# Optimization experiments

Measured on AMD Instinct MI355X. Metric: run time of the kernel, lower is better.

## Reference

```python
import jax, jax.numpy as jnp
import numpy as np

M, N, T = 32, 32, 512
H1 = (M + N) * 10 * 8      # 5120
H2 = M * N * 4             # 4096
HID = 1000                 # GRU hidden (hardcoded in module)
EPS = 1e-12


def _l2norm(x):
    # torch.nn.functional.normalize: x / max(||x||_2, eps)
    return x / jnp.maximum(jnp.linalg.norm(x), EPS)


def setup_inputs() -> dict:
    key = jax.random.key(0)
    ks = jax.random.split(key, 16)
    rn = lambda k, shp, s: (jax.random.normal(k, shp, dtype=jnp.float32) * s)
    inp = {
        "y": rn(ks[0], (T, N), 1.0),
        "F": rn(ks[1], (M, M), 0.5 / np.sqrt(M)),   # stable dynamics
        "H": rn(ks[2], (N, M), 1.0 / np.sqrt(M)),
        "m1x0": rn(ks[3], (M,), 1.0),
        "h0": rn(ks[4], (HID,), 1.0),
        "W1": rn(ks[5], (H1, M + N), 1.0 / np.sqrt(M + N)),
        "b1": rn(ks[6], (H1,), 0.01),
        "Wih": rn(ks[7], (3 * HID, H1), 1.0 / np.sqrt(H1)),
        "bih": rn(ks[8], (3 * HID,), 0.01),
        "Whh": rn(ks[9], (3 * HID, HID), 1.0 / np.sqrt(HID)),
        "bhh": rn(ks[10], (3 * HID,), 0.01),
        "W2": rn(ks[11], (H2, HID), 1.0 / np.sqrt(HID)),
        "b2": rn(ks[12], (H2,), 0.01),
        "W3": rn(ks[13], (M * N, H2), 1.0 / np.sqrt(H2)),
        "b3": rn(ks[14], (M * N,), 0.01),
    }
    return inp


def reference(y, F, H, m1x0, h0, W1, b1, Wih, bih, Whh, bhh, W2, b2, W3, b3):
    m, n = F.shape[0], H.shape[0]

    def step(carry, yt):
        m1x_prior, m1x_post, h = carry
        # step_prior
        m1x_prev_prior = m1x_prior
        m1x_prior = F @ m1x_post              # [m]
        m1y = H @ m1x_prior                   # [n]
        # step_KGain_est: features
        dm1x_n = _l2norm(m1x_post - m1x_prev_prior)
        dm1y_n = _l2norm(yt - m1y)
        kin = jnp.concatenate([dm1y_n, dm1x_n])  # [n+m]
        # KGain_step: Linear+ReLU -> single-step GRU -> Linear+ReLU -> Linear
        x = jax.nn.relu(W1 @ kin + b1)        # [H1]
        gi = Wih @ x + bih                    # [3*HID]
        gh = Whh @ h + bhh
        ir, iz, ic = jnp.split(gi, 3)
        hr, hz, hc = jnp.split(gh, 3)
        r = jax.nn.sigmoid(ir + hr)
        z = jax.nn.sigmoid(iz + hz)
        c = jnp.tanh(ic + r * hc)
        h_new = (1.0 - z) * c + z * h         # GRU hidden [HID]
        l2 = jax.nn.relu(W2 @ h_new + b2)     # [H2]
        KG = (W3 @ l2 + b3).reshape(m, n)     # Kalman gain
        # KNet_step: innovation update
        m1x_post_new = m1x_prior + KG @ (yt - m1y)
        return (m1x_prior, m1x_post_new, h_new), m1x_post_new

    init = (m1x0, m1x0, h0)
    _, posts = jax.lax.scan(step, init, y)
    return posts  # [T, m]
```

## Files before the change

### kernel.cpp

```cpp
#include <hip/hip_runtime.h>
#include <cmath>

#define Mdim 32
#define Ndim 32
#define Tsteps 512
#define H1dim 5120
#define H2dim 4096
#define HIDdim 1000
#define NWG 256
#define NTHR 1024
#define POLLER 320

typedef unsigned int u32;
typedef unsigned short u16;
typedef unsigned int u32x4 __attribute__((ext_vector_type(4)));

__device__ u16 g_w2b[H2dim * HIDdim];
__device__ u16 g_w3t[H2dim * Mdim * Ndim];

#define OFF_WIH 0
#define OFF_WHH 122880
#define OFF_UNION 146880
#define OFF_H9 157120
#define OFF_MISC 161640
#define SMEM_BYTES 162560

#define MI_POST 0
#define MI_PRIOR 32
#define MI_INNOV 96
#define MI_KIN 128
#define MI_GI 192
#define MI_GH 204

#define BAR_ARR(g) ((g) * 32)
#define BAR_L2 1024
#define BAR_GO(g) (2048 + (g) * 32)

__device__ __forceinline__ u16 f2bf(float f) {
  u32 u = __float_as_uint(f);
  return (u16)((u + 0x7fffu + ((u >> 16) & 1u)) >> 16);
}
__device__ __forceinline__ float bflo(u32 u) { return __uint_as_float(u << 16); }
__device__ __forceinline__ float bfhi(u32 u) { return __uint_as_float(u & 0xffff0000u); }

__device__ __forceinline__ float dot4(float4 a, float4 b) {
  return a.x * b.x + a.y * b.y + a.z * b.z + a.w * b.w;
}
__device__ __forceinline__ float dot8_bb(uint4 a, uint4 b) {
  float s = 0.f;
  s = fmaf(bflo(a.x), bflo(b.x), s); s = fmaf(bfhi(a.x), bfhi(b.x), s);
  s = fmaf(bflo(a.y), bflo(b.y), s); s = fmaf(bfhi(a.y), bfhi(b.y), s);
  s = fmaf(bflo(a.z), bflo(b.z), s); s = fmaf(bfhi(a.z), bfhi(b.z), s);
  s = fmaf(bflo(a.w), bflo(b.w), s); s = fmaf(bfhi(a.w), bfhi(b.w), s);
  return s;
}
__device__ __forceinline__ float dot8_bf(uint4 a, const float* x8) {
  float s = 0.f;
  s = fmaf(bflo(a.x), x8[0], s); s = fmaf(bfhi(a.x), x8[1], s);
  s = fmaf(bflo(a.y), x8[2], s); s = fmaf(bfhi(a.y), x8[3], s);
  s = fmaf(bflo(a.z), x8[4], s); s = fmaf(bfhi(a.z), x8[5], s);
  s = fmaf(bflo(a.w), x8[6], s); s = fmaf(bfhi(a.w), x8[7], s);
  return s;
}

__device__ __forceinline__ float wave_reduce64(float v) {
#pragma unroll
  for (int off = 32; off >= 1; off >>= 1) v += __shfl_xor(v, off, 64);
  return v;
}

__device__ __forceinline__ uint4 ldg_cg4u(const void* p) {
  uint4 r;
  asm volatile("global_load_dwordx4 %0, %1, off sc0 sc1\n\ts_waitcnt vmcnt(0)"
               : "=v"(r) : "v"(p) : "memory");
  return r;
}
__device__ __forceinline__ void stg_cg4u(void* p, u32 a, u32 b, u32 c, u32 d) {
  u32x4 v; v.x = a; v.y = b; v.z = c; v.w = d;
  asm volatile("global_store_dwordx4 %0, %1, off sc0 sc1" :: "v"(p), "v"(v) : "memory");
}
__device__ __forceinline__ void stg_cg1u(u32* p, u32 v) {
  asm volatile("global_store_dword %0, %1, off sc0 sc1" :: "v"(p), "v"(v) : "memory");
}
__device__ __forceinline__ float ldg_sum16_cg(const float* p) {
  float r0, r1, r2, r3, r4, r5, r6, r7, r8, r9, r10, r11, r12, r13, r14, r15;
  asm volatile(
      "global_load_dword %0, %16, off sc0 sc1\n\t"
      "global_load_dword %1, %16, off offset:128 sc0 sc1\n\t"
      "global_load_dword %2, %16, off offset:256 sc0 sc1\n\t"
      "global_load_dword %3, %16, off offset:384 sc0 sc1\n\t"
      "global_load_dword %4, %16, off offset:512 sc0 sc1\n\t"
      "global_load_dword %5, %16, off offset:640 sc0 sc1\n\t"
      "global_load_dword %6, %16, off offset:768 sc0 sc1\n\t"
      "global_load_dword %7, %16, off offset:896 sc0 sc1\n\t"
      "global_load_dword %8, %16, off offset:1024 sc0 sc1\n\t"
      "global_load_dword %9, %16, off offset:1152 sc0 sc1\n\t"
      "global_load_dword %10, %16, off offset:1280 sc0 sc1\n\t"
      "global_load_dword %11, %16, off offset:1408 sc0 sc1\n\t"
      "global_load_dword %12, %16, off offset:1536 sc0 sc1\n\t"
      "global_load_dword %13, %16, off offset:1664 sc0 sc1\n\t"
      "global_load_dword %14, %16, off offset:1792 sc0 sc1\n\t"
      "global_load_dword %15, %16, off offset:1920 sc0 sc1\n\t"
      "s_waitcnt vmcnt(0)"
      : "=&v"(r0), "=&v"(r1), "=&v"(r2), "=&v"(r3), "=&v"(r4), "=&v"(r5),
        "=&v"(r6), "=&v"(r7), "=&v"(r8), "=&v"(r9), "=&v"(r10), "=&v"(r11),
        "=&v"(r12), "=&v"(r13), "=&v"(r14), "=&v"(r15)
      : "v"(p) : "memory");
  return (((r0 + r1) + (r2 + r3)) + ((r4 + r5) + (r6 + r7))) +
         (((r8 + r9) + (r10 + r11)) + ((r12 + r13) + (r14 + r15)));
}

__device__ __forceinline__ void gb_arrive(u32* bar, u32 nb) {
  asm volatile("s_waitcnt vmcnt(0)" ::: "memory");
  __syncthreads();
  if (threadIdx.x == POLLER) {
    u32 g = (u32)blockIdx.x & 15u;
    u32 a = __hip_atomic_fetch_add(bar + BAR_ARR(g), 1u, __ATOMIC_RELAXED,
                                   __HIP_MEMORY_SCOPE_AGENT);
    if ((a & 15u) == 15u) {
      u32 b = __hip_atomic_fetch_add(bar + BAR_L2, 1u, __ATOMIC_RELAXED,
                                     __HIP_MEMORY_SCOPE_AGENT);
      if ((b & 15u) == 15u) {
#pragma unroll
        for (int gg = 0; gg < 16; ++gg) stg_cg1u(bar + BAR_GO(gg), nb);
      }
    }
  }
}
__device__ __forceinline__ void gb_wait(u32* bar, u32 nb) {
  if (threadIdx.x == POLLER) {
    u32* go = bar + BAR_GO((u32)blockIdx.x & 15u);
    while (__hip_atomic_load(go, __ATOMIC_RELAXED, __HIP_MEMORY_SCOPE_AGENT) < nb)
      __builtin_amdgcn_s_sleep(1);
  }
  __syncthreads();
}

__global__ void convert_w2(const float* __restrict__ W2) {
  int i = blockIdx.x * 1024 + threadIdx.x;
  if (i < H2dim * HIDdim) g_w2b[i] = f2bf(W2[i]);
}

__global__ void convert_w3t(const float* __restrict__ W3) {
  __shared__ float tile[32][33];
  int tr = blockIdx.x >> 7;
  int tc = blockIdx.x & 127;
  int r0 = tr * 32, c0 = tc * 32;
  int j = threadIdx.x & 31, i0 = threadIdx.x >> 5;
#pragma unroll
  for (int p = 0; p < 4; ++p) {
    int i = i0 + p * 8;
    tile[i][j] = W3[(size_t)(r0 + i) * H2dim + c0 + j];
  }
  __syncthreads();
#pragma unroll
  for (int p = 0; p < 4; ++p) {
    int i = i0 + p * 8;
    g_w3t[(size_t)(c0 + i) * 1024 + r0 + j] = f2bf(tile[j][i]);
  }
}

__global__ void __launch_bounds__(NTHR)
knet_kernel(const float* __restrict__ y, const float* __restrict__ F,
            const float* __restrict__ Hm, const float* __restrict__ m1x0,
            const float* __restrict__ h0, const float* __restrict__ W1,
            const float* __restrict__ b1, const float* __restrict__ Wih,
            const float* __restrict__ bih, const float* __restrict__ Whh,
            const float* __restrict__ bhh, const float* __restrict__ b2,
            const float* __restrict__ b3, float* __restrict__ out,
            u32* bar, u32* xbt, u32* hbt, float* acc) {
  extern __shared__ char smem[];
  u16* s_wih = (u16*)(smem + OFF_WIH);
  u16* s_whh = (u16*)(smem + OFF_WHH);
  u16* s_x = (u16*)(smem + OFF_UNION);
  float* s_pd = (float*)(smem + OFF_UNION);
  float* s_h9 = (float*)(smem + OFF_H9);
  float* s_m = (float*)(smem + OFF_MISC);
  float* s_post = s_m + MI_POST;
  float* s_prior = s_m + MI_PRIOR;
  float* s_innov = s_m + MI_INNOV;
  float* s_kin = s_m + MI_KIN;
  float* s_gi = s_m + MI_GI;
  float* s_gh = s_m + MI_GH;

  const int tid = threadIdx.x;
  const int w = tid >> 6;
  const int lane = tid & 63;
  const int wg = blockIdx.x;
  const int k0 = wg * 4;
  const bool gru_wg = (wg < 250);
  u32 nb = 0;

  if (gru_wg) {
#pragma unroll 1
    for (int r = 0; r < 12; ++r) {
      const float* src = Wih + (size_t)((r >> 2) * HIDdim + k0 + (r & 3)) * H1dim;
      u16* dst = s_wih + r * H1dim;
      for (int e = tid; e < H1dim; e += NTHR) dst[e] = f2bf(src[e]);
    }
#pragma unroll 1
    for (int r = 0; r < 12; ++r) {
      const float* src = Whh + (size_t)((r >> 2) * HIDdim + k0 + (r & 3)) * HIDdim;
      u16* dst = s_whh + r * HIDdim;
      for (int e = tid; e < HIDdim; e += NTHR) dst[e] = f2bf(src[e]);
    }
  }
  if (tid < 250) {
    float4 hv = ((const float4*)h0)[tid];
    int b0 = tid * 4;
    s_h9[((b0 + 0) >> 3) * 9 + ((b0 + 0) & 7)] = hv.x;
    s_h9[((b0 + 1) >> 3) * 9 + ((b0 + 1) & 7)] = hv.y;
    s_h9[((b0 + 2) >> 3) * 9 + ((b0 + 2) & 7)] = hv.z;
    s_h9[((b0 + 3) >> 3) * 9 + ((b0 + 3) & 7)] = hv.w;
  }
  __syncthreads();

  const int c2 = wg * 16 + w;
  float prior = 0.f, bb = 0.f, yv = 0.f;
  if (w == 0 && lane < 32) {
    prior = m1x0[lane];
    yv = y[lane];
  }

  auto gh_compute = [&]() {
    int base = (w - 12) * 3;
#pragma unroll
    for (int rr = 0; rr < 3; ++rr) {
      int r = base + rr;
      const uint4* wr = (const uint4*)(s_whh + r * HIDdim);
      float acc_ = dot8_bf(wr[lane], s_h9 + lane * 9);
      if (lane < 61) acc_ += dot8_bf(wr[lane + 64], s_h9 + (lane + 64) * 9);
      acc_ = wave_reduce64(acc_);
      if (lane == 0) s_gh[r] = acc_ + bhh[(r >> 2) * HIDdim + k0 + (r & 3)];
    }
  };
  if (gru_wg && w >= 12) gh_compute();

  for (int t = 0; t < Tsteps; ++t) {
    const u32 want = (u32)(t + 1);
    const int parR = (t + 1) & 1;
    const int parW = t & 1;
    if (w == 0) {
      float p = 0.f, inn = 0.f;
      float prev = prior;
      if (lane < 32) {
        if (t == 0) {
          p = m1x0[lane];
        } else {
          float d = ldg_sum16_cg(acc + parR * 512 + lane);
          p = prior + d + bb;
          if (wg == 0) out[(t - 1) * Mdim + lane] = p;
        }
        s_post[lane] = p;
      }
      asm volatile("" ::: "memory");
      if (lane < 32) {
        const float4* Fr = (const float4*)(F + lane * Mdim);
        const float4* pp = (const float4*)s_post;
        float s = 0.f;
#pragma unroll
        for (int j = 0; j < 8; ++j) s += dot4(Fr[j], pp[j]);
        prior = s;
        s_prior[lane] = s;
      }
      asm volatile("" ::: "memory");
      if (lane < 32) {
        const float4* Hr = (const float4*)(Hm + lane * Mdim);
        const float4* pp = (const float4*)s_prior;
        float s = 0.f;
#pragma unroll
        for (int j = 0; j < 8; ++j) s += dot4(Hr[j], pp[j]);
        inn = yv - s;
        s_innov[lane] = inn;
      }
      float vd = __shfl(p, lane & 31, 64) - __shfl(prev, lane & 31, 64);
      float v = (lane < 32) ? inn : vd;
      float sq = v * v;
#pragma unroll
      for (int off = 16; off >= 1; off >>= 1) sq += __shfl_xor(sq, off, 32);
      s_kin[lane] = v / fmaxf(sqrtf(sq), 1e-12f);
    }
    __syncthreads();

    if (w == 0) {
      int r = lane / 3;
      int p = lane - r * 3;
      float acc_ = 0.f;
      if (r < 20) {
        const float4* Wr = (const float4*)W1 + (size_t)(wg * 20 + r) * 16;
        const float4* kc = (const float4*)s_kin;
#pragma unroll
        for (int c = p; c < 16; c += 3) acc_ += dot4(Wr[c], kc[c]);
      }
      int rr = (r < 20) ? r : 0;
      float a1v = __shfl(acc_, rr * 3 + 1, 64);
      float a2v = __shfl(acc_, rr * 3 + 2, 64);
      u32 myval = 0;
      if (r < 20 && p == 0)
        myval = (u32)f2bf(fmaxf(acc_ + a1v + a2v + b1[wg * 20 + r], 0.f));
      u32 vs[7];
      int q = (lane < 3) ? lane : 0;
#pragma unroll
      for (int s2 = 0; s2 < 7; ++s2) {
        int ridx = q * 7 + s2;
        vs[s2] = __shfl(myval, (ridx < 20 ? ridx : 0) * 3, 64);
      }
      if (lane < 3) {
        stg_cg4u((char*)xbt + (size_t)(wg * 3 + lane) * 16,
                 vs[0] | (vs[1] << 16),
                 vs[2] | (vs[3] << 16),
                 vs[4] | (vs[5] << 16),
                 ((lane == 2) ? 0u : vs[6]) | (want << 16));
      }
    }
    float u;
    uint4 w2a, w2b_;
    {
      const uint4* tr3 = (const uint4*)(g_w3t + (size_t)c2 * 1024);
      uint4 t0 = tr3[2 * lane], t1 = tr3[2 * lane + 1];
      const float* iv = s_innov + 16 * (lane & 1);
      u = dot8_bf(t0, iv) + dot8_bf(t1, iv + 8);
      u += __shfl_xor(u, 1, 64);
      const uint4* w2p = (const uint4*)(g_w2b + (size_t)c2 * HIDdim);
      w2a = w2p[lane];
      w2b_ = (lane < 61) ? w2p[lane + 64] : make_uint4(0u, 0u, 0u, 0u);
    }
    if (gru_wg && tid >= 256) {
      int g = tid - 256;
      int swg = g / 3;
      int q = g - swg * 3;
      const char* gp = (const char*)xbt + (size_t)g * 16;
      uint4 v;
      for (;;) {
        v = ldg_cg4u(gp);
        if ((v.w >> 16) == want) break;
        __builtin_amdgcn_s_sleep(1);
      }
      u16* sx = (u16*)s_x;
      int base = swg * 20 + q * 7;
      sx[base + 0] = (u16)(v.x & 0xffff);
      sx[base + 1] = (u16)(v.x >> 16);
      sx[base + 2] = (u16)(v.y & 0xffff);
      sx[base + 3] = (u16)(v.y >> 16);
      sx[base + 4] = (u16)(v.z & 0xffff);
      sx[base + 5] = (u16)(v.z >> 16);
      if (q != 2) sx[base + 6] = (u16)(v.w & 0xffff);
    }
    __syncthreads();

    if (wg == 0 && tid < 128)
      stg_cg4u(acc + parR * 512 + tid * 4, 0u, 0u, 0u, 0u);

    if (gru_wg && w < 12) {
      const uint4* wr = (const uint4*)(s_wih + w * H1dim);
      const uint4* xr = (const uint4*)s_x;
      float acc_ = 0.f;
#pragma unroll
      for (int i = 0; i < 10; ++i) {
        int j = lane + 64 * i;
        acc_ += dot8_bb(wr[j], xr[j]);
      }
      acc_ = wave_reduce64(acc_);
      if (lane == 0) s_gi[w] = acc_ + bih[(w >> 2) * HIDdim + k0 + (w & 3)];
    }
    __syncthreads();

    if (gru_wg && w == 0 && lane < 4) {
      int k = k0 + lane;
      float hold = s_h9[(k >> 3) * 9 + (k & 7)];
      float ir = s_gi[lane], iz = s_gi[4 + lane], ic = s_gi[8 + lane];
      float r = 1.f / (1.f + expf(-(ir + s_gh[lane])));
      float z = 1.f / (1.f + expf(-(iz + s_gh[4 + lane])));
      float c_ = tanhf(ic + r * s_gh[8 + lane]);
      float hv = (1.f - z) * c_ + z * hold;
      stg_cg4u((char*)hbt + (size_t)k * 16, __float_as_uint(hv), want, 0u, 0u);
    }
    if (tid < HIDdim) {
      const char* gp = (const char*)hbt + (size_t)tid * 16;
      uint4 v;
      for (;;) {
        v = ldg_cg4u(gp);
        if (v.y == want) break;
        __builtin_amdgcn_s_sleep(1);
      }
      s_h9[(tid >> 3) * 9 + (tid & 7)] = __uint_as_float(v.x);
    }
    __syncthreads();

    {
      float acc_ = dot8_bf(w2a, s_h9 + lane * 9);
      if (lane < 61) acc_ += dot8_bf(w2b_, s_h9 + (lane + 64) * 9);
      acc_ = wave_reduce64(acc_);
      float l2c = fmaxf(acc_ + b2[c2], 0.f);
      if ((lane & 1) == 0) s_pd[w * 32 + (lane >> 1)] = l2c * u;
    }
    __syncthreads();
    if (tid < 32) {
      float pdv = 0.f;
#pragma unroll
      for (int ww = 0; ww < 16; ++ww) pdv += s_pd[ww * 32 + tid];
      __hip_atomic_fetch_add(acc + parW * 512 + (wg & 15) * 32 + tid, pdv,
                             __ATOMIC_RELAXED, __HIP_MEMORY_SCOPE_AGENT);
    }
    ++nb;
    gb_arrive(bar, nb);
    if (gru_wg && w >= 12) gh_compute();
    if (w == 0 && lane < 32) {
      int tn = (t + 1 < Tsteps) ? t + 1 : Tsteps - 1;
      yv = y[tn * Ndim + lane];
      float b = 0.f;
#pragma unroll 8
      for (int j = 0; j < 32; ++j) b = fmaf(b3[lane * 32 + j], s_innov[j], b);
      bb = b;
    }
    gb_wait(bar, nb);
  }

  if (wg == 0 && w == 0 && lane < 32) {
    float d = ldg_sum16_cg(acc + ((Tsteps - 1) & 1) * 512 + lane);
    out[(Tsteps - 1) * Mdim + lane] = prior + d + bb;
  }
}

extern "C" void kernel_launch(void* const* d_in, const int* in_sizes, int n_in,
                              void* d_out, int out_size, void* d_ws, size_t ws_size,
                              hipStream_t stream) {
  const float* y    = (const float*)d_in[0];
  const float* F    = (const float*)d_in[1];
  const float* Hm   = (const float*)d_in[2];
  const float* m1x0 = (const float*)d_in[3];
  const float* h0   = (const float*)d_in[4];
  const float* W1   = (const float*)d_in[5];
  const float* b1   = (const float*)d_in[6];
  const float* Wih  = (const float*)d_in[7];
  const float* bih  = (const float*)d_in[8];
  const float* Whh  = (const float*)d_in[9];
  const float* bhh  = (const float*)d_in[10];
  const float* W2   = (const float*)d_in[11];
  const float* b2   = (const float*)d_in[12];
  const float* W3   = (const float*)d_in[13];
  const float* b3   = (const float*)d_in[14];
  float* out = (float*)d_out;

  u32* bar   = (u32*)d_ws;
  float* acc = (float*)((char*)d_ws + 16384);
  u32* xbt   = (u32*)((char*)d_ws + 20480);
  u32* hbt   = (u32*)((char*)d_ws + 32768);

  convert_w2<<<4000, 1024, 0, stream>>>(W2);
  convert_w3t<<<4096, 256, 0, stream>>>(W3);
  hipMemsetAsync(d_ws, 0, 49152, stream);
  hipFuncSetAttribute((const void*)knet_kernel,
                      hipFuncAttributeMaxDynamicSharedMemorySize, SMEM_BYTES);
  void* args[] = {&y, &F, &Hm, &m1x0, &h0, &W1, &b1, &Wih, &bih, &Whh, &bhh,
                  &b2, &b3, &out, &bar, &xbt, &hbt, &acc};
  hipLaunchCooperativeKernel((const void*)knet_kernel, dim3(NWG), dim3(NTHR),
                             args, SMEM_BYTES, stream);
}
```

Measured before the change: 6.062 ms.

## Replace two-level atomic grid barrier with single sweeper workgroup polling counters

The grid barrier drops the second-level atomic counter. Each workgroup now makes one atomic increment on its group counter, and a dedicated workgroup (255) repeatedly sums all 16 counters and then broadcasts the go flags. Non-sweeper pollers keep two loads in flight so the release is seen sooner, and the sleeps inside the data-readiness spin loops are removed. This is meant to shorten the serial atomic chain on each of the 512 steps. In exchange the sweeper's own barrier wait gets longer and memory traffic from busy-polling rises.

```diff
diff --git a/kernel.cpp b/kernel.cpp
--- a/kernel.cpp
+++ b/kernel.cpp
@@ -10,6 +10,7 @@
 #define NWG 256
 #define NTHR 1024
 #define POLLER 320
+#define SWEEP_WG 255
 
 typedef unsigned int u32;
 typedef unsigned short u16;
@@ -33,7 +34,6 @@
 #define MI_GH 204
 
 #define BAR_ARR(g) ((g) * 32)
-#define BAR_L2 1024
 #define BAR_GO(g) (2048 + (g) * 32)
 
 __device__ __forceinline__ u16 f2bf(float f) {
@@ -81,6 +81,9 @@
 }
 __device__ __forceinline__ void stg_cg1u(u32* p, u32 v) {
   asm volatile("global_store_dword %0, %1, off sc0 sc1" :: "v"(p), "v"(v) : "memory");
+}
+__device__ __forceinline__ void ld1_issue(u32& r, const u32* p) {
+  asm volatile("global_load_dword %0, %1, off sc0 sc1" : "=v"(r) : "v"(p) : "memory");
 }
 __device__ __forceinline__ float ldg_sum16_cg(const float* p) {
   float r0, r1, r2, r3, r4, r5, r6, r7, r8, r9, r10, r11, r12, r13, r14, r15;
@@ -109,29 +112,66 @@
   return (((r0 + r1) + (r2 + r3)) + ((r4 + r5) + (r6 + r7))) +
          (((r8 + r9) + (r10 + r11)) + ((r12 + r13) + (r14 + r15)));
 }
-
-__device__ __forceinline__ void gb_arrive(u32* bar, u32 nb) {
+__device__ __forceinline__ u32 ldg_sum16u(const u32* p) {
+  u32 r0, r1, r2, r3, r4, r5, r6, r7, r8, r9, r10, r11, r12, r13, r14, r15;
+  asm volatile(
+      "global_load_dword %0, %16, off sc0 sc1\n\t"
+      "global_load_dword %1, %16, off offset:128 sc0 sc1\n\t"
+      "global_load_dword %2, %16, off offset:256 sc0 sc1\n\t"
+      "global_load_dword %3, %16, off offset:384 sc0 sc1\n\t"
+      "global_load_dword %4, %16, off offset:512 sc0 sc1\n\t"
+      "global_load_dword %5, %16, off offset:640 sc0 sc1\n\t"
+      "global_load_dword %6, %16, off offset:768 sc0 sc1\n\t"
+      "global_load_dword %7, %16, off offset:896 sc0 sc1\n\t"
+      "global_load_dword %8, %16, off offset:1024 sc0 sc1\n\t"
+      "global_load_dword %9, %16, off offset:1152 sc0 sc1\n\t"
+      "global_load_dword %10, %16, off offset:1280 sc0 sc1\n\t"
+      "global_load_dword %11, %16, off offset:1408 sc0 sc1\n\t"
+      "global_load_dword %12, %16, off offset:1536 sc0 sc1\n\t"
+      "global_load_dword %13, %16, off offset:1664 sc0 sc1\n\t"
+      "global_load_dword %14, %16, off offset:1792 sc0 sc1\n\t"
+      "global_load_dword %15, %16, off offset:1920 sc0 sc1\n\t"
+      "s_waitcnt vmcnt(0)"
+      : "=&v"(r0), "=&v"(r1), "=&v"(r2), "=&v"(r3), "=&v"(r4), "=&v"(r5),
+        "=&v"(r6), "=&v"(r7), "=&v"(r8), "=&v"(r9), "=&v"(r10), "=&v"(r11),
+        "=&v"(r12), "=&v"(r13), "=&v"(r14), "=&v"(r15)
+      : "v"(p) : "memory");
+  return (((r0 + r1) + (r2 + r3)) + ((r4 + r5) + (r6 + r7))) +
+         (((r8 + r9) + (r10 + r11)) + ((r12 + r13) + (r14 + r15)));
+}
+
+__device__ __forceinline__ void gb_arrive(u32* bar) {
   asm volatile("s_waitcnt vmcnt(0)" ::: "memory");
   __syncthreads();
-  if (threadIdx.x == POLLER) {
-    u32 g = (u32)blockIdx.x & 15u;
-    u32 a = __hip_atomic_fetch_add(bar + BAR_ARR(g), 1u, __ATOMIC_RELAXED,
-                                   __HIP_MEMORY_SCOPE_AGENT);
-    if ((a & 15u) == 15u) {
-      u32 b = __hip_atomic_fetch_add(bar + BAR_L2, 1u, __ATOMIC_RELAXED,
-                                     __HIP_MEMORY_SCOPE_AGENT);
-      if ((b & 15u) == 15u) {
-#pragma unroll
-        for (int gg = 0; gg < 16; ++gg) stg_cg1u(bar + BAR_GO(gg), nb);
-      }
-    }
-  }
+  if (threadIdx.x == POLLER)
+    __hip_atomic_fetch_add(bar + BAR_ARR((u32)blockIdx.x & 15u), 1u,
+                           __ATOMIC_RELAXED, __HIP_MEMORY_SCOPE_AGENT);
 }
 __device__ __forceinline__ void gb_wait(u32* bar, u32 nb) {
   if (threadIdx.x == POLLER) {
-    u32* go = bar + BAR_GO((u32)blockIdx.x & 15u);
-    while (__hip_atomic_load(go, __ATOMIC_RELAXED, __HIP_MEMORY_SCOPE_AGENT) < nb)
-      __builtin_amdgcn_s_sleep(1);
+    if (blockIdx.x == SWEEP_WG) {
+      const u32 target = nb * (u32)NWG;
+      while (ldg_sum16u(bar + BAR_ARR(0)) < target) {  }
+#pragma unroll
+      for (int gg = 0; gg < 16; ++gg) stg_cg1u(bar + BAR_GO(gg), nb);
+    } else {
+      u32* go = bar + BAR_GO((u32)blockIdx.x & 15u);
+      u32 g0, g1;
+      ld1_issue(g0, go);
+      for (;;) {
+        __builtin_amdgcn_s_sleep(1);
+        ld1_issue(g1, go);
+        asm volatile("s_waitcnt vmcnt(1)" ::: "memory");
+        __builtin_amdgcn_sched_barrier(0);
+        if (g0 >= nb) break;
+        __builtin_amdgcn_s_sleep(1);
+        ld1_issue(g0, go);
+        asm volatile("s_waitcnt vmcnt(1)" ::: "memory");
+        __builtin_amdgcn_sched_barrier(0);
+        if (g1 >= nb) break;
+      }
+      asm volatile("s_waitcnt vmcnt(0)" ::: "memory");
+    }
   }
   __syncthreads();
 }
@@ -334,7 +374,6 @@
       for (;;) {
         v = ldg_cg4u(gp);
         if ((v.w >> 16) == want) break;
-        __builtin_amdgcn_s_sleep(1);
       }
       u16* sx = (u16*)s_x;
       int base = swg * 20 + q * 7;
@@ -381,7 +420,6 @@
       for (;;) {
         v = ldg_cg4u(gp);
         if (v.y == want) break;
-        __builtin_amdgcn_s_sleep(1);
       }
       s_h9[(tid >> 3) * 9 + (tid & 7)] = __uint_as_float(v.x);
     }
@@ -403,7 +441,7 @@
                              __ATOMIC_RELAXED, __HIP_MEMORY_SCOPE_AGENT);
     }
     ++nb;
-    gb_arrive(bar, nb);
+    gb_arrive(bar);
     if (gru_wg && w >= 12) gh_compute();
     if (w == 0 && lane < 32) {
       int tn = (t + 1 < Tsteps) ? t + 1 : Tsteps - 1;
```

New measurement: 6.099 ms. About the same (+0.6%).
